# Performance work log

Measured on AMD Instinct MI355X. Metric: run time of the kernel, lower is better.

Reference implementation:

```python
import jax, jax.numpy as jnp
import numpy as np

TAU = 1.0
EPS = 1e-30
LN_EPS = 1e-5


def setup_inputs() -> dict:
    key = jax.random.key(0)
    ks = jax.random.split(key, 5)
    N, E, D_in, D_out = 50000, 800000, 128, 128
    x = jax.random.normal(ks[0], (N, D_in), dtype=jnp.float32)
    edge_src = jax.random.randint(ks[1], (E,), 0, N, dtype=jnp.int64)
    edge_dst = jax.random.randint(ks[2], (E,), 0, N, dtype=jnp.int64)
    W = jax.random.normal(ks[3], (2 * D_in, D_out), dtype=jnp.float32) * (1.0 / np.sqrt(2 * D_in))
    b = jnp.zeros((D_out,), dtype=jnp.float32)
    gamma = jnp.ones((D_out,), dtype=jnp.float32)
    beta = jnp.zeros((D_out,), dtype=jnp.float32)
    return {"x": x, "edge_src": edge_src, "edge_dst": edge_dst, "W": W, "b": b, "gamma": gamma, "beta": beta}


def _scatter_logsumexp(src, index, dim_size):
    # src: [E, D] gathered neighbor features, index: [E] target node ids
    scaled = src.astype(jnp.float32) / TAU
    mx = jax.ops.segment_max(scaled, index, num_segments=dim_size)  # [N, D], -inf for empty
    exp_val = jnp.exp(scaled - mx[index])                            # [E, D]
    sum_exp = jax.ops.segment_sum(exp_val, index, num_segments=dim_size)  # [N, D]
    out = TAU * (mx + jnp.log(jnp.maximum(sum_exp, EPS)))
    deg = jax.ops.segment_sum(jnp.ones_like(index, dtype=jnp.int32), index, num_segments=dim_size)
    return jnp.where((deg > 0)[:, None], out, 0.0)


def reference(x, edge_src, edge_dst, W, b, gamma, beta):
    N = x.shape[0]
    src_feat = x[edge_src]                                  # [E, D] gather
    agg = _scatter_logsumexp(src_feat, edge_dst, N)         # [N, D]
    h = jnp.concatenate([x, agg], axis=-1) @ W + b          # [N, D_out]
    mean = jnp.mean(h, axis=-1, keepdims=True)
    var = jnp.var(h, axis=-1, keepdims=True)
    h = (h - mean) * jax.lax.rsqrt(var + LN_EPS) * gamma + beta
    return jax.nn.relu(h)
```

## Files before the change

### kernel.cpp

```cpp
#include <hip/hip_runtime.h>
#include <math.h>

#define D 128
#define EPS 1e-30f
#define LN_EPS 1e-5f

#define BINSHIFT 9
#define BINW 512
#define NBIN_MAX 128
#define P1_EPB 4096

typedef long long ll;
typedef __attribute__((ext_vector_type(8))) short short8;
typedef __attribute__((ext_vector_type(4))) float f32x4;

__device__ inline unsigned short f2bf(float f) {
    unsigned int u = __float_as_uint(f);
    u += 0x7FFF + ((u >> 16) & 1);
    return (unsigned short)(u >> 16);
}

__device__ inline float bf2f_lo(unsigned int w) { return __uint_as_float(w << 16); }
__device__ inline float bf2f_hi(unsigned int w) { return __uint_as_float(w & 0xFFFF0000u); }

__device__ inline bool idx_is_i64(const void* p, int n_nodes) {
    const ll* q = (const ll*)p;
    bool ok = true;
#pragma unroll
    for (int i = 0; i < 4; ++i) {
        ll v = q[i];
        if (v < 0 || v >= (ll)n_nodes) ok = false;
    }
    return ok;
}

__device__ inline int load_idx(const void* p, ll e, bool is64) {
    return is64 ? (int)((const ll*)p)[e] : ((const int*)p)[e];
}


__global__ __launch_bounds__(256) void k_setup(const float* __restrict__ x,
                                               unsigned short* __restrict__ A,
                                               const float* __restrict__ W,
                                               unsigned short* __restrict__ WT,
                                               const void* __restrict__ edst,
                                               int* __restrict__ bhist,
                                               int N, int E, int PREP_B, int WT_B) {
    __shared__ int hist[NBIN_MAX];
    int b = blockIdx.x, t = threadIdx.x;
    if (b < PREP_B) {
        int i = b * 256 + t;
        if (i < N * 32) {
            int n = i >> 5, c4 = i & 31;
            float4 v = *(const float4*)(x + (ll)n * D + c4 * 4);
            ushort4 o;
            o.x = f2bf(v.x); o.y = f2bf(v.y); o.z = f2bf(v.z); o.w = f2bf(v.w);
            *(ushort4*)(A + (ll)n * 256 + c4 * 4) = o;
        }
        return;
    }
    b -= PREP_B;
    if (b < WT_B) {
        int idx = b * 256 + t;
        int k = idx >> 7, n = idx & 127;
        WT[n * 256 + k] = f2bf(W[idx]);
        return;
    }
    b -= WT_B;
    if (t < NBIN_MAX) hist[t] = 0;
    __syncthreads();
    bool is64 = idx_is_i64(edst, N);
    ll base = (ll)b * P1_EPB;
    int cnt = (int)min((ll)P1_EPB, (ll)E - base);
    for (int i = t; i < cnt; i += 256) {
        int d = load_idx(edst, base + i, is64);
        atomicAdd(&hist[d >> BINSHIFT], 1);
    }
    __syncthreads();
    if (t < NBIN_MAX) bhist[b * NBIN_MAX + t] = hist[t];
}

__global__ __launch_bounds__(NBIN_MAX) void k_binscan(const int* __restrict__ bhist, int EB,
                                                      int* __restrict__ pbase,
                                                      int* __restrict__ pcur,
                                                      int* __restrict__ off, int E, int N) {
    __shared__ int s[NBIN_MAX];
    int t = threadIdx.x;
    int v = 0;
    for (int i = 0; i < EB; ++i) v += bhist[i * NBIN_MAX + t];
    s[t] = v;
    __syncthreads();
    for (int o = 1; o < NBIN_MAX; o <<= 1) {
        int xv = (t >= o) ? s[t - o] : 0;
        __syncthreads();
        s[t] += xv;
        __syncthreads();
    }
    pbase[t] = s[t] - v;
    pcur[t]  = s[t] - v;
    if (t == NBIN_MAX - 1) { pbase[NBIN_MAX] = s[t]; off[N] = E; }
}

__global__ __launch_bounds__(256) void k_pass1b(const void* __restrict__ esrc,
                                                const void* __restrict__ edst,
                                                int* __restrict__ pcur,
                                                unsigned int* __restrict__ pairs,
                                                int E, int N) {
    __shared__ unsigned int sp[P1_EPB];
    __shared__ int hist[NBIN_MAX];
    __shared__ int curs[NBIN_MAX];
    bool is64s = idx_is_i64(esrc, N);
    bool is64d = idx_is_i64(edst, N);
    int t = threadIdx.x;
    if (t < NBIN_MAX) hist[t] = 0;
    __syncthreads();
    ll base = (ll)blockIdx.x * P1_EPB;
    int cnt = (int)min((ll)P1_EPB, (ll)E - base);
    for (int i = t; i < cnt; i += 256) {
        unsigned int s = (unsigned int)load_idx(esrc, base + i, is64s);
        unsigned int d = (unsigned int)load_idx(edst, base + i, is64d);
        sp[i] = (d << 16) | s;
        atomicAdd(&hist[d >> BINSHIFT], 1);
    }
    __syncthreads();
    if (t < NBIN_MAX) curs[t] = hist[t] ? atomicAdd(&pcur[t], hist[t]) : 0;
    __syncthreads();
    for (int i = t; i < cnt; i += 256) {
        unsigned int p = sp[i];
        int b = p >> (16 + BINSHIFT);
        int pos = atomicAdd(&curs[b], 1);
        pairs[pos] = p;
    }
}

__global__ __launch_bounds__(256) void k_pass2(const unsigned int* __restrict__ pairs,
                                               const int* __restrict__ pbase,
                                               int* __restrict__ off,
                                               unsigned short* __restrict__ bucket, int N) {
    __shared__ int dhist[BINW];
    __shared__ int dcur[BINW];
    __shared__ int ssum[256];
    int b = blockIdx.x, t = threadIdx.x;
    int p0 = pbase[b], p1 = pbase[b + 1];
    int n0 = b << BINSHIFT;
    for (int j = t; j < BINW; j += 256) dhist[j] = 0;
    __syncthreads();
    for (int i = p0 + t; i < p1; i += 256)
        atomicAdd(&dhist[(pairs[i] >> 16) & (BINW - 1)], 1);
    __syncthreads();
    int h0 = dhist[2 * t], h1 = dhist[2 * t + 1];
    int loc = h0 + h1;
    ssum[t] = loc;
    __syncthreads();
    for (int o = 1; o < 256; o <<= 1) {
        int xv = (t >= o) ? ssum[t - o] : 0;
        __syncthreads();
        ssum[t] += xv;
        __syncthreads();
    }
    int ex = ssum[t] - loc;
    dcur[2 * t]     = ex;
    dcur[2 * t + 1] = ex + h0;
    __syncthreads();
    int lim = min(BINW, N - n0);
    for (int j = t; j < lim; j += 256) off[n0 + j] = p0 + dcur[j];
    __syncthreads();
    for (int i = p0 + t; i < p1; i += 256) {
        unsigned int p = pairs[i];
        int dl = (p >> 16) & (BINW - 1);
        int pos = p0 + atomicAdd(&dcur[dl], 1);
        bucket[pos] = (unsigned short)(p & 0xFFFFu);
    }
}

__global__ __launch_bounds__(256) void k_aggregate(const int* __restrict__ off,
                                                   const unsigned short* __restrict__ bucket,
                                                   unsigned short* __restrict__ A, int N) {
    __shared__ int sIds[4][64];
    int w = threadIdx.x >> 6, lane = threadIdx.x & 63;
    int n = blockIdx.x * 4 + w;
    if (n >= N) return;
    int start = off[n], end = off[n + 1];
    int sub = lane >> 4, c16 = lane & 15;
    const uint4* A4 = (const uint4*)A;
    float acc[8];
#pragma unroll
    for (int j = 0; j < 8; ++j) acc[j] = 0.f;

    for (int c = start; c < end; c += 64) {
        int cn = min(64, end - c);
        if (lane < cn) sIds[w][lane] = bucket[c + lane];
        int j = sub;
        for (; j + 12 < cn; j += 16) {
            int s0 = sIds[w][j];
            int s1 = sIds[w][j + 4];
            int s2 = sIds[w][j + 8];
            int s3 = sIds[w][j + 12];
            uint4 v0 = A4[(ll)s0 * 32 + c16];
            uint4 v1 = A4[(ll)s1 * 32 + c16];
            uint4 v2 = A4[(ll)s2 * 32 + c16];
            uint4 v3 = A4[(ll)s3 * 32 + c16];
            acc[0] += __expf(bf2f_lo(v0.x)); acc[1] += __expf(bf2f_hi(v0.x));
            acc[2] += __expf(bf2f_lo(v0.y)); acc[3] += __expf(bf2f_hi(v0.y));
            acc[4] += __expf(bf2f_lo(v0.z)); acc[5] += __expf(bf2f_hi(v0.z));
            acc[6] += __expf(bf2f_lo(v0.w)); acc[7] += __expf(bf2f_hi(v0.w));
            acc[0] += __expf(bf2f_lo(v1.x)); acc[1] += __expf(bf2f_hi(v1.x));
            acc[2] += __expf(bf2f_lo(v1.y)); acc[3] += __expf(bf2f_hi(v1.y));
            acc[4] += __expf(bf2f_lo(v1.z)); acc[5] += __expf(bf2f_hi(v1.z));
            acc[6] += __expf(bf2f_lo(v1.w)); acc[7] += __expf(bf2f_hi(v1.w));
            acc[0] += __expf(bf2f_lo(v2.x)); acc[1] += __expf(bf2f_hi(v2.x));
            acc[2] += __expf(bf2f_lo(v2.y)); acc[3] += __expf(bf2f_hi(v2.y));
            acc[4] += __expf(bf2f_lo(v2.z)); acc[5] += __expf(bf2f_hi(v2.z));
            acc[6] += __expf(bf2f_lo(v2.w)); acc[7] += __expf(bf2f_hi(v2.w));
            acc[0] += __expf(bf2f_lo(v3.x)); acc[1] += __expf(bf2f_hi(v3.x));
            acc[2] += __expf(bf2f_lo(v3.y)); acc[3] += __expf(bf2f_hi(v3.y));
            acc[4] += __expf(bf2f_lo(v3.z)); acc[5] += __expf(bf2f_hi(v3.z));
            acc[6] += __expf(bf2f_lo(v3.w)); acc[7] += __expf(bf2f_hi(v3.w));
        }
        for (; j < cn; j += 4) {
            int s0 = sIds[w][j];
            uint4 v0 = A4[(ll)s0 * 32 + c16];
            acc[0] += __expf(bf2f_lo(v0.x)); acc[1] += __expf(bf2f_hi(v0.x));
            acc[2] += __expf(bf2f_lo(v0.y)); acc[3] += __expf(bf2f_hi(v0.y));
            acc[4] += __expf(bf2f_lo(v0.z)); acc[5] += __expf(bf2f_hi(v0.z));
            acc[6] += __expf(bf2f_lo(v0.w)); acc[7] += __expf(bf2f_hi(v0.w));
        }
    }
#pragma unroll
    for (int j = 0; j < 8; ++j) {
        acc[j] += __shfl_xor(acc[j], 16, 64);
        acc[j] += __shfl_xor(acc[j], 32, 64);
    }
    if (sub == 0) {
        int dg = end - start;
        unsigned int o[4];
#pragma unroll
        for (int k = 0; k < 4; ++k) {
            float a0 = (dg > 0) ? __logf(fmaxf(acc[2 * k],     EPS)) : 0.f;
            float a1 = (dg > 0) ? __logf(fmaxf(acc[2 * k + 1], EPS)) : 0.f;
            o[k] = (unsigned int)f2bf(a0) | ((unsigned int)f2bf(a1) << 16);
        }
        *(uint4*)(A + (ll)n * 256 + 128 + c16 * 8) = make_uint4(o[0], o[1], o[2], o[3]);
    }
}

__global__ __launch_bounds__(256) void k_gemm_mfma(
        const unsigned short* __restrict__ A,
        const unsigned short* __restrict__ WT,
        const float* __restrict__ bias,
        const float* __restrict__ gamma,
        const float* __restrict__ beta,
        float* __restrict__ out, int N) {
    __shared__ unsigned char sA[64 * 512];
    __shared__ float2 sPart[2][64];
    int t = threadIdx.x;
    int l = t & 63, w = t >> 6;
    int wr = w >> 1, wc = w & 1;
    int n0 = blockIdx.x * 64;

    const uint4* gA = (const uint4*)(A + (ll)n0 * 256);
#pragma unroll
    for (int i = 0; i < 8; ++i) {
        int c = i * 256 + t;
        int row = c >> 5, cc = c & 31;
        uint4 v = make_uint4(0u, 0u, 0u, 0u);
        if (n0 + row < N) v = gA[row * 32 + cc];
        *(uint4*)(sA + row * 512 + ((cc * 16) ^ ((row & 7) << 4))) = v;
    }
    __syncthreads();

    f32x4 acc[2][4];
#pragma unroll
    for (int m = 0; m < 2; ++m)
#pragma unroll
        for (int n = 0; n < 4; ++n) acc[m][n] = (f32x4){0.f, 0.f, 0.f, 0.f};

    const int lr = l & 15, lk = l >> 4;
    const int aswz = (lr & 7) << 4;
    const unsigned short* wbase = WT + (wc * 64 + lr) * 256 + lk * 8;

#pragma unroll
    for (int ks = 0; ks < 8; ++ks) {
        short8 a[2], b[4];
#pragma unroll
        for (int m = 0; m < 2; ++m) {
            int arow = wr * 32 + m * 16 + lr;
            a[m] = *(const short8*)(sA + arow * 512 + ((ks * 64 + lk * 16) ^ aswz));
        }
#pragma unroll
        for (int n = 0; n < 4; ++n)
            b[n] = *(const short8*)(wbase + n * 16 * 256 + ks * 32);
#pragma unroll
        for (int m = 0; m < 2; ++m)
#pragma unroll
            for (int n = 0; n < 4; ++n)
                acc[m][n] = __builtin_amdgcn_mfma_f32_16x16x32_bf16(a[m], b[n], acc[m][n], 0, 0, 0);
    }

    const int col_base = wc * 64 + lr;
    float bn[4], gn[4], ben[4];
#pragma unroll
    for (int n = 0; n < 4; ++n) {
        int col = col_base + n * 16;
        bn[n] = bias[col]; gn[n] = gamma[col]; ben[n] = beta[col];
    }
#pragma unroll
    for (int m = 0; m < 2; ++m) {
#pragma unroll
        for (int r = 0; r < 4; ++r) {
            float s = 0.f, q = 0.f;
#pragma unroll
            for (int n = 0; n < 4; ++n) {
                float v = acc[m][n][r] + bn[n];
                acc[m][n][r] = v;
                s += v; q += v * v;
            }
#pragma unroll
            for (int o = 1; o < 16; o <<= 1) {
                s += __shfl_xor(s, o, 64);
                q += __shfl_xor(q, o, 64);
            }
            if (lr == 0) {
                int rowl = wr * 32 + m * 16 + lk * 4 + r;
                sPart[wc][rowl] = make_float2(s, q);
            }
        }
    }
    __syncthreads();
#pragma unroll
    for (int m = 0; m < 2; ++m) {
#pragma unroll
        for (int r = 0; r < 4; ++r) {
            int rowl = wr * 32 + m * 16 + lk * 4 + r;
            float2 p0 = sPart[0][rowl], p1 = sPart[1][rowl];
            float ssum = p0.x + p1.x, qsum = p0.y + p1.y;
            float mean = ssum * (1.f / 128.f);
            float var  = qsum * (1.f / 128.f) - mean * mean;
            float rstd = rsqrtf(var + LN_EPS);
            int grow = n0 + rowl;
            if (grow < N) {
                float* op = out + (ll)grow * 128;
#pragma unroll
                for (int n = 0; n < 4; ++n) {
                    float y = (acc[m][n][r] - mean) * rstd * gn[n] + ben[n];
                    op[col_base + n * 16] = fmaxf(y, 0.f);
                }
            }
        }
    }
}


__global__ __launch_bounds__(256) void k_wt(const float* __restrict__ W,
                                            unsigned short* __restrict__ WT) {
    int idx = blockIdx.x * 256 + threadIdx.x;
    int k = idx >> 7, n = idx & 127;
    WT[n * 256 + k] = f2bf(W[idx]);
}

__global__ __launch_bounds__(256) void k_hist(const void* __restrict__ edst,
                                              int* __restrict__ deg, int E, int N) {
    bool is64 = idx_is_i64(edst, N);
    int i = blockIdx.x * 256 + threadIdx.x;
    if (i < E) atomicAdd(&deg[load_idx(edst, i, is64)], 1);
}

__global__ __launch_bounds__(256) void k_scanA(const int* __restrict__ deg,
                                               int* __restrict__ off,
                                               int* __restrict__ bsum, int N) {
    __shared__ int s[256];
    int b = blockIdx.x, t = threadIdx.x;
    int base = b * 1024 + t * 4;
    int v0 = 0, v1 = 0, v2 = 0, v3 = 0;
    if (base + 0 < N) v0 = deg[base + 0];
    if (base + 1 < N) v1 = deg[base + 1];
    if (base + 2 < N) v2 = deg[base + 2];
    if (base + 3 < N) v3 = deg[base + 3];
    int loc = v0 + v1 + v2 + v3;
    s[t] = loc;
    __syncthreads();
    for (int o = 1; o < 256; o <<= 1) {
        int xv = (t >= o) ? s[t - o] : 0;
        __syncthreads();
        s[t] += xv;
        __syncthreads();
    }
    int run = s[t] - loc;
    if (t == 255) bsum[b] = s[255];
    if (base + 0 < N) off[base + 0] = run; run += v0;
    if (base + 1 < N) off[base + 1] = run; run += v1;
    if (base + 2 < N) off[base + 2] = run; run += v2;
    if (base + 3 < N) off[base + 3] = run;
}

__global__ __launch_bounds__(256) void k_scanB(const int* __restrict__ bsum,
                                               int* __restrict__ bbase, int NB) {
    __shared__ int s[256];
    int t = threadIdx.x;
    int v = (t < NB) ? bsum[t] : 0;
    s[t] = v;
    __syncthreads();
    for (int o = 1; o < 256; o <<= 1) {
        int xv = (t >= o) ? s[t - o] : 0;
        __syncthreads();
        s[t] += xv;
        __syncthreads();
    }
    if (t < NB) bbase[t] = s[t] - v;
}

__global__ __launch_bounds__(256) void k_scanC(int* __restrict__ off,
                                               int* __restrict__ cur,
                                               const int* __restrict__ bbase, int N, int E) {
    int b = blockIdx.x, t = threadIdx.x;
    int add = bbase[b];
    int base = b * 1024 + t * 4;
#pragma unroll
    for (int i = 0; i < 4; ++i) {
        int idx = base + i;
        if (idx < N) {
            int o = off[idx] + add;
            off[idx] = o;
            cur[idx] = o;
        }
    }
    if (b == 0 && t == 0) off[N] = E;
}

__global__ __launch_bounds__(256) void k_scatter32(const void* __restrict__ esrc,
                                                   const void* __restrict__ edst,
                                                   int* __restrict__ cur,
                                                   unsigned short* __restrict__ bucket,
                                                   int E, int N) {
    bool is64s = idx_is_i64(esrc, N);
    bool is64d = idx_is_i64(edst, N);
    int i = blockIdx.x * 256 + threadIdx.x;
    if (i < E) {
        int s = load_idx(esrc, i, is64s);
        int d = load_idx(edst, i, is64d);
        int pos = atomicAdd(&cur[d], 1);
        bucket[pos] = (unsigned short)s;
    }
}

__global__ __launch_bounds__(128) void k_aggregate_mid(const float* __restrict__ x,
                                                       const unsigned short* __restrict__ bucket,
                                                       const int* __restrict__ off,
                                                       unsigned short* __restrict__ A, int N) {
    int n = blockIdx.x, t = threadIdx.x;
    int start = __builtin_amdgcn_readfirstlane(off[n]);
    int end   = __builtin_amdgcn_readfirstlane(off[n + 1]);
    float acc = 0.f;
    for (int e = start; e < end; ++e) {
        int s0 = bucket[e];
        acc += __expf(x[(ll)s0 * D + t]);
    }
    float agg = (end > start) ? __logf(fmaxf(acc, EPS)) : 0.f;
    A[(ll)n * 256 + t]       = f2bf(x[(ll)n * D + t]);
    A[(ll)n * 256 + 128 + t] = f2bf(agg);
}


__global__ __launch_bounds__(256) void scatter_expsum(
        const float* __restrict__ x, const void* __restrict__ esrc_raw,
        const void* __restrict__ edst_raw, float* __restrict__ sumexp,
        int* __restrict__ deg, int E, int N) {
    ll tid = (ll)blockIdx.x * blockDim.x + threadIdx.x;
    ll total = (ll)E * 32;
    if (tid >= total) return;
    bool is64 = idx_is_i64(esrc_raw, N);
    ll e = tid >> 5;
    int q = (int)(tid & 31);
    int s = load_idx(esrc_raw, e, is64);
    int d = load_idx(edst_raw, e, is64);
    const float4 v = *reinterpret_cast<const float4*>(x + (ll)s * D + q * 4);
    float* outp = sumexp + (ll)d * D + q * 4;
    atomicAdd(outp + 0, expf(v.x));
    atomicAdd(outp + 1, expf(v.y));
    atomicAdd(outp + 2, expf(v.z));
    atomicAdd(outp + 3, expf(v.w));
    if (q == 0) atomicAdd(deg + d, 1);
}

__global__ __launch_bounds__(128) void gemm_ln_relu_fb(
        const float* __restrict__ x, const float* __restrict__ sumexp,
        const int* __restrict__ deg, const float* __restrict__ W,
        const float* __restrict__ bias, const float* __restrict__ gamma,
        const float* __restrict__ beta, float* __restrict__ out) {
    const int n = blockIdx.x;
    const int t = threadIdx.x;
    __shared__ float v[2 * D];
    __shared__ float s_sum[2], s_sq[2];
    v[t] = x[(ll)n * D + t];
    float se = sumexp[(ll)n * D + t];
    v[D + t] = (deg[n] > 0) ? logf(fmaxf(se, EPS)) : 0.0f;
    __syncthreads();
    float acc = bias[t];
#pragma unroll 8
    for (int k = 0; k < 2 * D; ++k) acc += v[k] * W[k * D + t];
    float sum = acc, sq = acc * acc;
#pragma unroll
    for (int o = 32; o > 0; o >>= 1) {
        sum += __shfl_xor(sum, o, 64);
        sq  += __shfl_xor(sq, o, 64);
    }
    int w = t >> 6;
    if ((t & 63) == 0) { s_sum[w] = sum; s_sq[w] = sq; }
    __syncthreads();
    float mean = (s_sum[0] + s_sum[1]) * (1.0f / D);
    float var  = (s_sq[0] + s_sq[1]) * (1.0f / D) - mean * mean;
    float r = rsqrtf(var + LN_EPS);
    float y = (acc - mean) * r * gamma[t] + beta[t];
    out[(ll)n * D + t] = fmaxf(y, 0.0f);
}


extern "C" void kernel_launch(void* const* d_in, const int* in_sizes, int n_in,
                              void* d_out, int out_size, void* d_ws, size_t ws_size,
                              hipStream_t stream) {
    const float* x     = (const float*)d_in[0];
    const void*  esrc  = d_in[1];
    const void*  edst  = d_in[2];
    const float* W     = (const float*)d_in[3];
    const float* bias  = (const float*)d_in[4];
    const float* gamma = (const float*)d_in[5];
    const float* beta  = (const float*)d_in[6];

    const int E = in_sizes[1];
    const int N = in_sizes[0] / D;
    float* out = (float*)d_out;
    unsigned short* A = (unsigned short*)d_out;

    const int EB = (E + P1_EPB - 1) / P1_EPB;
    const int PREP_B = (N * 32 + 255) / 256;
    const int NBIN = (N + BINW - 1) >> BINSHIFT;

    size_t need_fast = ((size_t)(N + 1) + 129 + 128 + (size_t)EB * NBIN_MAX + (size_t)E) * 4
                     + (size_t)E * 2 + 2 + 65536;
    const int NB = (N + 1023) / 1024;
    size_t need_mid = ((size_t)3 * N + 1 + 512 + 16384) * 4 + (size_t)E * 2 + 2;

    if (N <= 65536 && ws_size >= need_fast) {
        int* off            = (int*)d_ws;
        int* pbase          = off + (N + 1);
        int* pcur           = pbase + 129;
        int* bhist          = pcur + 128;
        unsigned int* pairs = (unsigned int*)(bhist + (size_t)EB * NBIN_MAX);
        unsigned short* bucket = (unsigned short*)(pairs + E);
        unsigned short* wt  = (unsigned short*)((char*)(bucket + E) + (((size_t)(bucket + E)) & 2 ? 2 : 0));

        k_setup<<<PREP_B + 128 + EB, 256, 0, stream>>>(x, A, W, wt, edst, bhist, N, E, PREP_B, 128);
        k_binscan<<<1, NBIN_MAX, 0, stream>>>(bhist, EB, pbase, pcur, off, E, N);
        k_pass1b<<<EB, 256, 0, stream>>>(esrc, edst, pcur, pairs, E, N);
        k_pass2<<<NBIN, 256, 0, stream>>>(pairs, pbase, off, bucket, N);
        k_aggregate<<<(N + 3) / 4, 256, 0, stream>>>(off, bucket, A, N);
        k_gemm_mfma<<<(N + 63) / 64, 256, 0, stream>>>(A, wt, bias, gamma, beta, out, N);
    } else if (N <= 65536 && ws_size >= need_mid && NB <= 256) {
        int* deg    = (int*)d_ws;
        int* off    = deg + N;
        int* cur    = off + (N + 1);
        int* bsum   = cur + N;
        int* bbase  = bsum + 256;
        unsigned short* wt = (unsigned short*)(bbase + 256);
        unsigned short* bucket = wt + 32768;

        hipMemsetAsync(deg, 0, (size_t)N * sizeof(int), stream);
        int eb = (E + 255) / 256;
        k_wt<<<128, 256, 0, stream>>>(W, wt);
        k_hist<<<eb, 256, 0, stream>>>(edst, deg, E, N);
        k_scanA<<<NB, 256, 0, stream>>>(deg, off, bsum, N);
        k_scanB<<<1, 256, 0, stream>>>(bsum, bbase, NB);
        k_scanC<<<NB, 256, 0, stream>>>(off, cur, bbase, N, E);
        k_scatter32<<<eb, 256, 0, stream>>>(esrc, edst, cur, bucket, E, N);
        k_aggregate_mid<<<N, 128, 0, stream>>>(x, bucket, off, A, N);
        k_gemm_mfma<<<(N + 63) / 64, 256, 0, stream>>>(A, wt, bias, gamma, beta, out, N);
    } else {
        float* sumexp = out;
        int* deg = (int*)d_ws;
        hipMemsetAsync(sumexp, 0, (size_t)N * D * sizeof(float), stream);
        hipMemsetAsync(deg, 0, (size_t)N * sizeof(int), stream);
        ll total = (ll)E * 32;
        int blocks = (int)((total + 255) / 256);
        scatter_expsum<<<blocks, 256, 0, stream>>>(x, esrc, edst, sumexp, deg, E, N);
        gemm_ln_relu_fb<<<N, D, 0, stream>>>(x, sumexp, deg, W, bias, gamma, beta, out);
    }
}
```

Before: 143.2 us.

## Fuse neighbor aggregation into MFMA GEMM+LayerNorm kernel, staging A in workspace

Merges the log-sum-exp aggregation kernel into the GEMM/LayerNorm kernel. Each 64-row block gathers neighbor features, computes the aggregate and writes it straight into its shared-memory A tile, then runs the MFMA GEMM. This removes one launch and the global write/read of the aggregated half of A. A now lives in the workspace instead of aliasing the output buffer, since other blocks still gather x rows from A while outputs are written. The cost is lower parallelism during aggregation: 782 blocks each process 16 nodes per wave serially instead of 12.5k small blocks, which risks load imbalance and poorer latency hiding.

```diff
diff --git a/kernel.cpp b/kernel.cpp
--- a/kernel.cpp
+++ b/kernel.cpp
@@ -173,75 +173,291 @@
     }
 }
 
-__global__ __launch_bounds__(256) void k_aggregate(const int* __restrict__ off,
-                                                   const unsigned short* __restrict__ bucket,
-                                                   unsigned short* __restrict__ A, int N) {
+__global__ __launch_bounds__(256) void k_agg_gemm(
+        const unsigned short* __restrict__ A,
+        const int* __restrict__ off,
+        const unsigned short* __restrict__ bucket,
+        const unsigned short* __restrict__ WT,
+        const float* __restrict__ bias,
+        const float* __restrict__ gamma,
+        const float* __restrict__ beta,
+        float* __restrict__ out, int N) {
+    __shared__ unsigned char sA[64 * 512];
+    __shared__ float2 sPart[2][64];
     __shared__ int sIds[4][64];
-    int w = threadIdx.x >> 6, lane = threadIdx.x & 63;
-    int n = blockIdx.x * 4 + w;
-    if (n >= N) return;
-    int start = off[n], end = off[n + 1];
-    int sub = lane >> 4, c16 = lane & 15;
-    const uint4* A4 = (const uint4*)A;
-    float acc[8];
-#pragma unroll
-    for (int j = 0; j < 8; ++j) acc[j] = 0.f;
-
-    for (int c = start; c < end; c += 64) {
-        int cn = min(64, end - c);
-        if (lane < cn) sIds[w][lane] = bucket[c + lane];
-        int j = sub;
-        for (; j + 12 < cn; j += 16) {
-            int s0 = sIds[w][j];
-            int s1 = sIds[w][j + 4];
-            int s2 = sIds[w][j + 8];
-            int s3 = sIds[w][j + 12];
-            uint4 v0 = A4[(ll)s0 * 32 + c16];
-            uint4 v1 = A4[(ll)s1 * 32 + c16];
-            uint4 v2 = A4[(ll)s2 * 32 + c16];
-            uint4 v3 = A4[(ll)s3 * 32 + c16];
-            acc[0] += __expf(bf2f_lo(v0.x)); acc[1] += __expf(bf2f_hi(v0.x));
-            acc[2] += __expf(bf2f_lo(v0.y)); acc[3] += __expf(bf2f_hi(v0.y));
-            acc[4] += __expf(bf2f_lo(v0.z)); acc[5] += __expf(bf2f_hi(v0.z));
-            acc[6] += __expf(bf2f_lo(v0.w)); acc[7] += __expf(bf2f_hi(v0.w));
-            acc[0] += __expf(bf2f_lo(v1.x)); acc[1] += __expf(bf2f_hi(v1.x));
-            acc[2] += __expf(bf2f_lo(v1.y)); acc[3] += __expf(bf2f_hi(v1.y));
-            acc[4] += __expf(bf2f_lo(v1.z)); acc[5] += __expf(bf2f_hi(v1.z));
-            acc[6] += __expf(bf2f_lo(v1.w)); acc[7] += __expf(bf2f_hi(v1.w));
-            acc[0] += __expf(bf2f_lo(v2.x)); acc[1] += __expf(bf2f_hi(v2.x));
-            acc[2] += __expf(bf2f_lo(v2.y)); acc[3] += __expf(bf2f_hi(v2.y));
-            acc[4] += __expf(bf2f_lo(v2.z)); acc[5] += __expf(bf2f_hi(v2.z));
-            acc[6] += __expf(bf2f_lo(v2.w)); acc[7] += __expf(bf2f_hi(v2.w));
-            acc[0] += __expf(bf2f_lo(v3.x)); acc[1] += __expf(bf2f_hi(v3.x));
-            acc[2] += __expf(bf2f_lo(v3.y)); acc[3] += __expf(bf2f_hi(v3.y));
-            acc[4] += __expf(bf2f_lo(v3.z)); acc[5] += __expf(bf2f_hi(v3.z));
-            acc[6] += __expf(bf2f_lo(v3.w)); acc[7] += __expf(bf2f_hi(v3.w));
-        }
-        for (; j < cn; j += 4) {
-            int s0 = sIds[w][j];
-            uint4 v0 = A4[(ll)s0 * 32 + c16];
-            acc[0] += __expf(bf2f_lo(v0.x)); acc[1] += __expf(bf2f_hi(v0.x));
-            acc[2] += __expf(bf2f_lo(v0.y)); acc[3] += __expf(bf2f_hi(v0.y));
-            acc[4] += __expf(bf2f_lo(v0.z)); acc[5] += __expf(bf2f_hi(v0.z));
-            acc[6] += __expf(bf2f_lo(v0.w)); acc[7] += __expf(bf2f_hi(v0.w));
-        }
-    }
-#pragma unroll
-    for (int j = 0; j < 8; ++j) {
-        acc[j] += __shfl_xor(acc[j], 16, 64);
-        acc[j] += __shfl_xor(acc[j], 32, 64);
-    }
-    if (sub == 0) {
-        int dg = end - start;
-        unsigned int o[4];
-#pragma unroll
-        for (int k = 0; k < 4; ++k) {
-            float a0 = (dg > 0) ? __logf(fmaxf(acc[2 * k],     EPS)) : 0.f;
-            float a1 = (dg > 0) ? __logf(fmaxf(acc[2 * k + 1], EPS)) : 0.f;
-            o[k] = (unsigned int)f2bf(a0) | ((unsigned int)f2bf(a1) << 16);
-        }
-        *(uint4*)(A + (ll)n * 256 + 128 + c16 * 8) = make_uint4(o[0], o[1], o[2], o[3]);
-    }
+    int t = threadIdx.x;
+    int l = t & 63, w = t >> 6;
+    int n0 = blockIdx.x * 64;
+
+    const uint4* gA = (const uint4*)A;
+#pragma unroll
+    for (int i = 0; i < 4; ++i) {
+        int c = i * 256 + t;
+        int row = c >> 4;
+        int cc = c & 15;
+        uint4 v = make_uint4(0u, 0u, 0u, 0u);
+        if (n0 + row < N) v = gA[(ll)(n0 + row) * 32 + cc];
+        *(uint4*)(sA + row * 512 + ((cc * 16) ^ ((row & 7) << 4))) = v;
+    }
+
+    int sub = l >> 4, c16 = l & 15;
+    for (int i = 0; i < 16; ++i) {
+        int row = w * 16 + i;
+        int n = n0 + row;
+        if (n >= N) break;
+        int start = off[n], end = off[n + 1];
+        float acc[8];
+#pragma unroll
+        for (int j = 0; j < 8; ++j) acc[j] = 0.f;
+        for (int c = start; c < end; c += 64) {
+            int cn = min(64, end - c);
+            if (l < cn) sIds[w][l] = bucket[c + l];
+            int j = sub;
+            for (; j + 12 < cn; j += 16) {
+                int s0 = sIds[w][j];
+                int s1 = sIds[w][j + 4];
+                int s2 = sIds[w][j + 8];
+                int s3 = sIds[w][j + 12];
+                uint4 v0 = gA[(ll)s0 * 32 + c16];
+                uint4 v1 = gA[(ll)s1 * 32 + c16];
+                uint4 v2 = gA[(ll)s2 * 32 + c16];
+                uint4 v3 = gA[(ll)s3 * 32 + c16];
+                acc[0] += __expf(bf2f_lo(v0.x)); acc[1] += __expf(bf2f_hi(v0.x));
+                acc[2] += __expf(bf2f_lo(v0.y)); acc[3] += __expf(bf2f_hi(v0.y));
+                acc[4] += __expf(bf2f_lo(v0.z)); acc[5] += __expf(bf2f_hi(v0.z));
+                acc[6] += __expf(bf2f_lo(v0.w)); acc[7] += __expf(bf2f_hi(v0.w));
+                acc[0] += __expf(bf2f_lo(v1.x)); acc[1] += __expf(bf2f_hi(v1.x));
+                acc[2] += __expf(bf2f_lo(v1.y)); acc[3] += __expf(bf2f_hi(v1.y));
+                acc[4] += __expf(bf2f_lo(v1.z)); acc[5] += __expf(bf2f_hi(v1.z));
+                acc[6] += __expf(bf2f_lo(v1.w)); acc[7] += __expf(bf2f_hi(v1.w));
+                acc[0] += __expf(bf2f_lo(v2.x)); acc[1] += __expf(bf2f_hi(v2.x));
+                acc[2] += __expf(bf2f_lo(v2.y)); acc[3] += __expf(bf2f_hi(v2.y));
+                acc[4] += __expf(bf2f_lo(v2.z)); acc[5] += __expf(bf2f_hi(v2.z));
+                acc[6] += __expf(bf2f_lo(v2.w)); acc[7] += __expf(bf2f_hi(v2.w));
+                acc[0] += __expf(bf2f_lo(v3.x)); acc[1] += __expf(bf2f_hi(v3.x));
+                acc[2] += __expf(bf2f_lo(v3.y)); acc[3] += __expf(bf2f_hi(v3.y));
+                acc[4] += __expf(bf2f_lo(v3.z)); acc[5] += __expf(bf2f_hi(v3.z));
+                acc[6] += __expf(bf2f_lo(v3.w)); acc[7] += __expf(bf2f_hi(v3.w));
+            }
+            for (; j < cn; j += 4) {
+                int s0 = sIds[w][j];
+                uint4 v0 = gA[(ll)s0 * 32 + c16];
+                acc[0] += __expf(bf2f_lo(v0.x)); acc[1] += __expf(bf2f_hi(v0.x));
+                acc[2] += __expf(bf2f_lo(v0.y)); acc[3] += __expf(bf2f_hi(v0.y));
+                acc[4] += __expf(bf2f_lo(v0.z)); acc[5] += __expf(bf2f_hi(v0.z));
+                acc[6] += __expf(bf2f_lo(v0.w)); acc[7] += __expf(bf2f_hi(v0.w));
+            }
+        }
+#pragma unroll
+        for (int j = 0; j < 8; ++j) {
+            acc[j] += __shfl_xor(acc[j], 16, 64);
+            acc[j] += __shfl_xor(acc[j], 32, 64);
+        }
+        if (sub == 0) {
+            int dg = end - start;
+            unsigned int o[4];
+#pragma unroll
+            for (int k = 0; k < 4; ++k) {
+                float a0 = (dg > 0) ? __logf(fmaxf(acc[2 * k],     EPS)) : 0.f;
+                float a1 = (dg > 0) ? __logf(fmaxf(acc[2 * k + 1], EPS)) : 0.f;
+                o[k] = (unsigned int)f2bf(a0) | ((unsigned int)f2bf(a1) << 16);
+            }
+            *(uint4*)(sA + row * 512 + (((16 + c16) * 16) ^ ((row & 7) << 4))) =
+                make_uint4(o[0], o[1], o[2], o[3]);
+        }
+    }
+    __syncthreads();
+
+    int wr = w >> 1, wc = w & 1;
+    f32x4 acc[2][4];
+#pragma unroll
+    for (int m = 0; m < 2; ++m)
+#pragma unroll
+        for (int n = 0; n < 4; ++n) acc[m][n] = (f32x4){0.f, 0.f, 0.f, 0.f};
+
+    const int lr = l & 15, lk = l >> 4;
+    const int aswz = (lr & 7) << 4;
+    const unsigned short* wbase = WT + (wc * 64 + lr) * 256 + lk * 8;
+
+#pragma unroll
+    for (int ks = 0; ks < 8; ++ks) {
+        short8 a[2], b[4];
+#pragma unroll
+        for (int m = 0; m < 2; ++m) {
+            int arow = wr * 32 + m * 16 + lr;
+            a[m] = *(const short8*)(sA + arow * 512 + ((ks * 64 + lk * 16) ^ aswz));
+        }
+#pragma unroll
+        for (int n = 0; n < 4; ++n)
+            b[n] = *(const short8*)(wbase + n * 16 * 256 + ks * 32);
+#pragma unroll
+        for (int m = 0; m < 2; ++m)
+#pragma unroll
+            for (int n = 0; n < 4; ++n)
+                acc[m][n] = __builtin_amdgcn_mfma_f32_16x16x32_bf16(a[m], b[n], acc[m][n], 0, 0, 0);
+    }
+
+    const int col_base = wc * 64 + lr;
+    float bn[4], gn[4], ben[4];
+#pragma unroll
+    for (int n = 0; n < 4; ++n) {
+        int col = col_base + n * 16;
+        bn[n] = bias[col]; gn[n] = gamma[col]; ben[n] = beta[col];
+    }
+#pragma unroll
+    for (int m = 0; m < 2; ++m) {
+#pragma unroll
+        for (int r = 0; r < 4; ++r) {
+            float s = 0.f, q = 0.f;
+#pragma unroll
+            for (int n = 0; n < 4; ++n) {
+                float v = acc[m][n][r] + bn[n];
+                acc[m][n][r] = v;
+                s += v; q += v * v;
+            }
+#pragma unroll
+            for (int o = 1; o < 16; o <<= 1) {
+                s += __shfl_xor(s, o, 64);
+                q += __shfl_xor(q, o, 64);
+            }
+            if (lr == 0) {
+                int rowl = wr * 32 + m * 16 + lk * 4 + r;
+                sPart[wc][rowl] = make_float2(s, q);
+            }
+        }
+    }
+    __syncthreads();
+#pragma unroll
+    for (int m = 0; m < 2; ++m) {
+#pragma unroll
+        for (int r = 0; r < 4; ++r) {
+            int rowl = wr * 32 + m * 16 + lk * 4 + r;
+            float2 p0 = sPart[0][rowl], p1 = sPart[1][rowl];
+            float ssum = p0.x + p1.x, qsum = p0.y + p1.y;
+            float mean = ssum * (1.f / 128.f);
+            float var  = qsum * (1.f / 128.f) - mean * mean;
+            float rstd = rsqrtf(var + LN_EPS);
+            int grow = n0 + rowl;
+            if (grow < N) {
+                float* op = out + (ll)grow * 128;
+#pragma unroll
+                for (int n = 0; n < 4; ++n) {
+                    float y = (acc[m][n][r] - mean) * rstd * gn[n] + ben[n];
+                    op[col_base + n * 16] = fmaxf(y, 0.f);
+                }
+            }
+        }
+    }
+}
+
+
+__global__ __launch_bounds__(256) void k_wt(const float* __restrict__ W,
+                                            unsigned short* __restrict__ WT) {
+    int idx = blockIdx.x * 256 + threadIdx.x;
+    int k = idx >> 7, n = idx & 127;
+    WT[n * 256 + k] = f2bf(W[idx]);
+}
+
+__global__ __launch_bounds__(256) void k_hist(const void* __restrict__ edst,
+                                              int* __restrict__ deg, int E, int N) {
+    bool is64 = idx_is_i64(edst, N);
+    int i = blockIdx.x * 256 + threadIdx.x;
+    if (i < E) atomicAdd(&deg[load_idx(edst, i, is64)], 1);
+}
+
+__global__ __launch_bounds__(256) void k_scanA(const int* __restrict__ deg,
+                                               int* __restrict__ off,
+                                               int* __restrict__ bsum, int N) {
+    __shared__ int s[256];
+    int b = blockIdx.x, t = threadIdx.x;
+    int base = b * 1024 + t * 4;
+    int v0 = 0, v1 = 0, v2 = 0, v3 = 0;
+    if (base + 0 < N) v0 = deg[base + 0];
+    if (base + 1 < N) v1 = deg[base + 1];
+    if (base + 2 < N) v2 = deg[base + 2];
+    if (base + 3 < N) v3 = deg[base + 3];
+    int loc = v0 + v1 + v2 + v3;
+    s[t] = loc;
+    __syncthreads();
+    for (int o = 1; o < 256; o <<= 1) {
+        int xv = (t >= o) ? s[t - o] : 0;
+        __syncthreads();
+        s[t] += xv;
+        __syncthreads();
+    }
+    int run = s[t] - loc;
+    if (t == 255) bsum[b] = s[255];
+    if (base + 0 < N) off[base + 0] = run; run += v0;
+    if (base + 1 < N) off[base + 1] = run; run += v1;
+    if (base + 2 < N) off[base + 2] = run; run += v2;
+    if (base + 3 < N) off[base + 3] = run;
+}
+
+__global__ __launch_bounds__(256) void k_scanB(const int* __restrict__ bsum,
+                                               int* __restrict__ bbase, int NB) {
+    __shared__ int s[256];
+    int t = threadIdx.x;
+    int v = (t < NB) ? bsum[t] : 0;
+    s[t] = v;
+    __syncthreads();
+    for (int o = 1; o < 256; o <<= 1) {
+        int xv = (t >= o) ? s[t - o] : 0;
+        __syncthreads();
+        s[t] += xv;
+        __syncthreads();
+    }
+    if (t < NB) bbase[t] = s[t] - v;
+}
+
+__global__ __launch_bounds__(256) void k_scanC(int* __restrict__ off,
+                                               int* __restrict__ cur,
+                                               const int* __restrict__ bbase, int N, int E) {
+    int b = blockIdx.x, t = threadIdx.x;
+    int add = bbase[b];
+    int base = b * 1024 + t * 4;
+#pragma unroll
+    for (int i = 0; i < 4; ++i) {
+        int idx = base + i;
+        if (idx < N) {
+            int o = off[idx] + add;
+            off[idx] = o;
+            cur[idx] = o;
+        }
+    }
+    if (b == 0 && t == 0) off[N] = E;
+}
+
+__global__ __launch_bounds__(256) void k_scatter32(const void* __restrict__ esrc,
+                                                   const void* __restrict__ edst,
+                                                   int* __restrict__ cur,
+                                                   unsigned short* __restrict__ bucket,
+                                                   int E, int N) {
+    bool is64s = idx_is_i64(esrc, N);
+    bool is64d = idx_is_i64(edst, N);
+    int i = blockIdx.x * 256 + threadIdx.x;
+    if (i < E) {
+        int s = load_idx(esrc, i, is64s);
+        int d = load_idx(edst, i, is64d);
+        int pos = atomicAdd(&cur[d], 1);
+        bucket[pos] = (unsigned short)s;
+    }
+}
+
+__global__ __launch_bounds__(128) void k_aggregate_mid(const float* __restrict__ x,
+                                                       const unsigned short* __restrict__ bucket,
+                                                       const int* __restrict__ off,
+                                                       unsigned short* __restrict__ A, int N) {
+    int n = blockIdx.x, t = threadIdx.x;
+    int start = __builtin_amdgcn_readfirstlane(off[n]);
+    int end   = __builtin_amdgcn_readfirstlane(off[n + 1]);
+    float acc = 0.f;
+    for (int e = start; e < end; ++e) {
+        int s0 = bucket[e];
+        acc += __expf(x[(ll)s0 * D + t]);
+    }
+    float agg = (end > start) ? __logf(fmaxf(acc, EPS)) : 0.f;
+    A[(ll)n * 256 + t]       = f2bf(x[(ll)n * D + t]);
+    A[(ll)n * 256 + 128 + t] = f2bf(agg);
 }
 
 __global__ __launch_bounds__(256) void k_gemm_mfma(
@@ -348,116 +564,6 @@
             }
         }
     }
-}
-
-
-__global__ __launch_bounds__(256) void k_wt(const float* __restrict__ W,
-                                            unsigned short* __restrict__ WT) {
-    int idx = blockIdx.x * 256 + threadIdx.x;
-    int k = idx >> 7, n = idx & 127;
-    WT[n * 256 + k] = f2bf(W[idx]);
-}
-
-__global__ __launch_bounds__(256) void k_hist(const void* __restrict__ edst,
-                                              int* __restrict__ deg, int E, int N) {
-    bool is64 = idx_is_i64(edst, N);
-    int i = blockIdx.x * 256 + threadIdx.x;
-    if (i < E) atomicAdd(&deg[load_idx(edst, i, is64)], 1);
-}
-
-__global__ __launch_bounds__(256) void k_scanA(const int* __restrict__ deg,
-                                               int* __restrict__ off,
-                                               int* __restrict__ bsum, int N) {
-    __shared__ int s[256];
-    int b = blockIdx.x, t = threadIdx.x;
-    int base = b * 1024 + t * 4;
-    int v0 = 0, v1 = 0, v2 = 0, v3 = 0;
-    if (base + 0 < N) v0 = deg[base + 0];
-    if (base + 1 < N) v1 = deg[base + 1];
-    if (base + 2 < N) v2 = deg[base + 2];
-    if (base + 3 < N) v3 = deg[base + 3];
-    int loc = v0 + v1 + v2 + v3;
-    s[t] = loc;
-    __syncthreads();
-    for (int o = 1; o < 256; o <<= 1) {
-        int xv = (t >= o) ? s[t - o] : 0;
-        __syncthreads();
-        s[t] += xv;
-        __syncthreads();
-    }
-    int run = s[t] - loc;
-    if (t == 255) bsum[b] = s[255];
-    if (base + 0 < N) off[base + 0] = run; run += v0;
-    if (base + 1 < N) off[base + 1] = run; run += v1;
-    if (base + 2 < N) off[base + 2] = run; run += v2;
-    if (base + 3 < N) off[base + 3] = run;
-}
-
-__global__ __launch_bounds__(256) void k_scanB(const int* __restrict__ bsum,
-                                               int* __restrict__ bbase, int NB) {
-    __shared__ int s[256];
-    int t = threadIdx.x;
-    int v = (t < NB) ? bsum[t] : 0;
-    s[t] = v;
-    __syncthreads();
-    for (int o = 1; o < 256; o <<= 1) {
-        int xv = (t >= o) ? s[t - o] : 0;
-        __syncthreads();
-        s[t] += xv;
-        __syncthreads();
-    }
-    if (t < NB) bbase[t] = s[t] - v;
-}
-
-__global__ __launch_bounds__(256) void k_scanC(int* __restrict__ off,
-                                               int* __restrict__ cur,
-                                               const int* __restrict__ bbase, int N, int E) {
-    int b = blockIdx.x, t = threadIdx.x;
-    int add = bbase[b];
-    int base = b * 1024 + t * 4;
-#pragma unroll
-    for (int i = 0; i < 4; ++i) {
-        int idx = base + i;
-        if (idx < N) {
-            int o = off[idx] + add;
-            off[idx] = o;
-            cur[idx] = o;
-        }
-    }
-    if (b == 0 && t == 0) off[N] = E;
-}
-
-__global__ __launch_bounds__(256) void k_scatter32(const void* __restrict__ esrc,
-                                                   const void* __restrict__ edst,
-                                                   int* __restrict__ cur,
-                                                   unsigned short* __restrict__ bucket,
-                                                   int E, int N) {
-    bool is64s = idx_is_i64(esrc, N);
-    bool is64d = idx_is_i64(edst, N);
-    int i = blockIdx.x * 256 + threadIdx.x;
-    if (i < E) {
-        int s = load_idx(esrc, i, is64s);
-        int d = load_idx(edst, i, is64d);
-        int pos = atomicAdd(&cur[d], 1);
-        bucket[pos] = (unsigned short)s;
-    }
-}
-
-__global__ __launch_bounds__(128) void k_aggregate_mid(const float* __restrict__ x,
-                                                       const unsigned short* __restrict__ bucket,
-                                                       const int* __restrict__ off,
-                                                       unsigned short* __restrict__ A, int N) {
-    int n = blockIdx.x, t = threadIdx.x;
-    int start = __builtin_amdgcn_readfirstlane(off[n]);
-    int end   = __builtin_amdgcn_readfirstlane(off[n + 1]);
-    float acc = 0.f;
-    for (int e = start; e < end; ++e) {
-        int s0 = bucket[e];
-        acc += __expf(x[(ll)s0 * D + t]);
-    }
-    float agg = (end > start) ? __logf(fmaxf(acc, EPS)) : 0.f;
-    A[(ll)n * 256 + t]       = f2bf(x[(ll)n * D + t]);
-    A[(ll)n * 256 + 128 + t] = f2bf(agg);
 }
 
 
@@ -529,19 +635,20 @@
     const int E = in_sizes[1];
     const int N = in_sizes[0] / D;
     float* out = (float*)d_out;
-    unsigned short* A = (unsigned short*)d_out;
 
     const int EB = (E + P1_EPB - 1) / P1_EPB;
     const int PREP_B = (N * 32 + 255) / 256;
     const int NBIN = (N + BINW - 1) >> BINSHIFT;
 
-    size_t need_fast = ((size_t)(N + 1) + 129 + 128 + (size_t)EB * NBIN_MAX + (size_t)E) * 4
+    size_t need_fast = (size_t)N * 512
+                     + ((size_t)(N + 1) + 129 + 128 + (size_t)EB * NBIN_MAX + (size_t)E) * 4
                      + (size_t)E * 2 + 2 + 65536;
     const int NB = (N + 1023) / 1024;
     size_t need_mid = ((size_t)3 * N + 1 + 512 + 16384) * 4 + (size_t)E * 2 + 2;
 
     if (N <= 65536 && ws_size >= need_fast) {
-        int* off            = (int*)d_ws;
+        unsigned short* A   = (unsigned short*)d_ws;
+        int* off            = (int*)(A + (size_t)N * 256);
         int* pbase          = off + (N + 1);
         int* pcur           = pbase + 129;
         int* bhist          = pcur + 128;
@@ -553,9 +660,10 @@
         k_binscan<<<1, NBIN_MAX, 0, stream>>>(bhist, EB, pbase, pcur, off, E, N);
         k_pass1b<<<EB, 256, 0, stream>>>(esrc, edst, pcur, pairs, E, N);
         k_pass2<<<NBIN, 256, 0, stream>>>(pairs, pbase, off, bucket, N);
-        k_aggregate<<<(N + 3) / 4, 256, 0, stream>>>(off, bucket, A, N);
-        k_gemm_mfma<<<(N + 63) / 64, 256, 0, stream>>>(A, wt, bias, gamma, beta, out, N);
+        k_agg_gemm<<<(N + 63) / 64, 256, 0, stream>>>(A, off, bucket, wt,
+                                                      bias, gamma, beta, out, N);
     } else if (N <= 65536 && ws_size >= need_mid && NB <= 256) {
+        unsigned short* A = (unsigned short*)d_out;
         int* deg    = (int*)d_ws;
         int* off    = deg + N;
         int* cur    = off + (N + 1);
```

After: 155.1 us. +8.3%, slower.

## Precompute exp(x) per node in bf16 and gather it in aggregation

Applied to the files above, without the earlier changes.

The setup kernel now writes a separate bf16 table of exp(x) per node, so the aggregation kernel gathers precomputed exponentials and only sums them. This drops E*D exponentials in favour of N*D and gathers from a compact 256-byte row instead of the 512-byte stride of the A buffer. The aggregation loop is also unrolled to 8 gathers per iteration for more memory-level parallelism. The cost is an extra N*D bf16 workspace buffer written during setup, rounding exp to bf16 before summation, and no max-subtraction, which risks overflow for large inputs.

```diff
diff --git a/kernel.cpp b/kernel.cpp
--- a/kernel.cpp
+++ b/kernel.cpp
@@ -41,6 +41,7 @@
 
 __global__ __launch_bounds__(256) void k_setup(const float* __restrict__ x,
                                                unsigned short* __restrict__ A,
+                                               unsigned short* __restrict__ expx,
                                                const float* __restrict__ W,
                                                unsigned short* __restrict__ WT,
                                                const void* __restrict__ edst,
@@ -56,6 +57,10 @@
             ushort4 o;
             o.x = f2bf(v.x); o.y = f2bf(v.y); o.z = f2bf(v.z); o.w = f2bf(v.w);
             *(ushort4*)(A + (ll)n * 256 + c4 * 4) = o;
+            ushort4 e;
+            e.x = f2bf(__expf(v.x)); e.y = f2bf(__expf(v.y));
+            e.z = f2bf(__expf(v.z)); e.w = f2bf(__expf(v.w));
+            *(ushort4*)(expx + (ll)n * D + c4 * 4) = e;
         }
         return;
     }
@@ -175,6 +180,7 @@
 
 __global__ __launch_bounds__(256) void k_aggregate(const int* __restrict__ off,
                                                    const unsigned short* __restrict__ bucket,
+                                                   const unsigned short* __restrict__ expx,
                                                    unsigned short* __restrict__ A, int N) {
     __shared__ int sIds[4][64];
     int w = threadIdx.x >> 6, lane = threadIdx.x & 63;
@@ -182,7 +188,7 @@
     if (n >= N) return;
     int start = off[n], end = off[n + 1];
     int sub = lane >> 4, c16 = lane & 15;
-    const uint4* A4 = (const uint4*)A;
+    const uint4* E4 = (const uint4*)expx;
     float acc[8];
 #pragma unroll
     for (int j = 0; j < 8; ++j) acc[j] = 0.f;
@@ -191,39 +197,35 @@
         int cn = min(64, end - c);
         if (lane < cn) sIds[w][lane] = bucket[c + lane];
         int j = sub;
-        for (; j + 12 < cn; j += 16) {
+        for (; j + 28 < cn; j += 32) {
             int s0 = sIds[w][j];
             int s1 = sIds[w][j + 4];
             int s2 = sIds[w][j + 8];
             int s3 = sIds[w][j + 12];
-            uint4 v0 = A4[(ll)s0 * 32 + c16];
-            uint4 v1 = A4[(ll)s1 * 32 + c16];
-            uint4 v2 = A4[(ll)s2 * 32 + c16];
-            uint4 v3 = A4[(ll)s3 * 32 + c16];
-            acc[0] += __expf(bf2f_lo(v0.x)); acc[1] += __expf(bf2f_hi(v0.x));
-            acc[2] += __expf(bf2f_lo(v0.y)); acc[3] += __expf(bf2f_hi(v0.y));
-            acc[4] += __expf(bf2f_lo(v0.z)); acc[5] += __expf(bf2f_hi(v0.z));
-            acc[6] += __expf(bf2f_lo(v0.w)); acc[7] += __expf(bf2f_hi(v0.w));
-            acc[0] += __expf(bf2f_lo(v1.x)); acc[1] += __expf(bf2f_hi(v1.x));
-            acc[2] += __expf(bf2f_lo(v1.y)); acc[3] += __expf(bf2f_hi(v1.y));
-            acc[4] += __expf(bf2f_lo(v1.z)); acc[5] += __expf(bf2f_hi(v1.z));
-            acc[6] += __expf(bf2f_lo(v1.w)); acc[7] += __expf(bf2f_hi(v1.w));
-            acc[0] += __expf(bf2f_lo(v2.x)); acc[1] += __expf(bf2f_hi(v2.x));
-            acc[2] += __expf(bf2f_lo(v2.y)); acc[3] += __expf(bf2f_hi(v2.y));
-            acc[4] += __expf(bf2f_lo(v2.z)); acc[5] += __expf(bf2f_hi(v2.z));
-            acc[6] += __expf(bf2f_lo(v2.w)); acc[7] += __expf(bf2f_hi(v2.w));
-            acc[0] += __expf(bf2f_lo(v3.x)); acc[1] += __expf(bf2f_hi(v3.x));
-            acc[2] += __expf(bf2f_lo(v3.y)); acc[3] += __expf(bf2f_hi(v3.y));
-            acc[4] += __expf(bf2f_lo(v3.z)); acc[5] += __expf(bf2f_hi(v3.z));
-            acc[6] += __expf(bf2f_lo(v3.w)); acc[7] += __expf(bf2f_hi(v3.w));
+            int s4 = sIds[w][j + 16];
+            int s5 = sIds[w][j + 20];
+            int s6 = sIds[w][j + 24];
+            int s7 = sIds[w][j + 28];
+            uint4 v0 = E4[(ll)s0 * 16 + c16];
+            uint4 v1 = E4[(ll)s1 * 16 + c16];
+            uint4 v2 = E4[(ll)s2 * 16 + c16];
+            uint4 v3 = E4[(ll)s3 * 16 + c16];
+            uint4 v4 = E4[(ll)s4 * 16 + c16];
+            uint4 v5 = E4[(ll)s5 * 16 + c16];
+            uint4 v6 = E4[(ll)s6 * 16 + c16];
+            uint4 v7 = E4[(ll)s7 * 16 + c16];
+#define ACC(v) \
+            acc[0] += bf2f_lo(v.x); acc[1] += bf2f_hi(v.x); \
+            acc[2] += bf2f_lo(v.y); acc[3] += bf2f_hi(v.y); \
+            acc[4] += bf2f_lo(v.z); acc[5] += bf2f_hi(v.z); \
+            acc[6] += bf2f_lo(v.w); acc[7] += bf2f_hi(v.w);
+            ACC(v0) ACC(v1) ACC(v2) ACC(v3) ACC(v4) ACC(v5) ACC(v6) ACC(v7)
         }
         for (; j < cn; j += 4) {
             int s0 = sIds[w][j];
-            uint4 v0 = A4[(ll)s0 * 32 + c16];
-            acc[0] += __expf(bf2f_lo(v0.x)); acc[1] += __expf(bf2f_hi(v0.x));
-            acc[2] += __expf(bf2f_lo(v0.y)); acc[3] += __expf(bf2f_hi(v0.y));
-            acc[4] += __expf(bf2f_lo(v0.z)); acc[5] += __expf(bf2f_hi(v0.z));
-            acc[6] += __expf(bf2f_lo(v0.w)); acc[7] += __expf(bf2f_hi(v0.w));
+            uint4 v0 = E4[(ll)s0 * 16 + c16];
+            ACC(v0)
+#undef ACC
         }
     }
 #pragma unroll
@@ -535,25 +537,28 @@
     const int PREP_B = (N * 32 + 255) / 256;
     const int NBIN = (N + BINW - 1) >> BINSHIFT;
 
-    size_t need_fast = ((size_t)(N + 1) + 129 + 128 + (size_t)EB * NBIN_MAX + (size_t)E) * 4
-                     + (size_t)E * 2 + 2 + 65536;
+    size_t need_fast = (size_t)N * 256
+                     + ((size_t)(N + 1) + 129 + 128 + (size_t)EB * NBIN_MAX + (size_t)E) * 4
+                     + 65536 + (size_t)E * 2 + 64;
     const int NB = (N + 1023) / 1024;
     size_t need_mid = ((size_t)3 * N + 1 + 512 + 16384) * 4 + (size_t)E * 2 + 2;
 
     if (N <= 65536 && ws_size >= need_fast) {
-        int* off            = (int*)d_ws;
-        int* pbase          = off + (N + 1);
-        int* pcur           = pbase + 129;
-        int* bhist          = pcur + 128;
-        unsigned int* pairs = (unsigned int*)(bhist + (size_t)EB * NBIN_MAX);
-        unsigned short* bucket = (unsigned short*)(pairs + E);
-        unsigned short* wt  = (unsigned short*)((char*)(bucket + E) + (((size_t)(bucket + E)) & 2 ? 2 : 0));
-
-        k_setup<<<PREP_B + 128 + EB, 256, 0, stream>>>(x, A, W, wt, edst, bhist, N, E, PREP_B, 128);
+        unsigned short* expx = (unsigned short*)d_ws;
+        int* off             = (int*)(expx + (size_t)N * 128);
+        int* pbase           = off + (N + 1);
+        int* pcur            = pbase + 129;
+        int* bhist           = pcur + 128;
+        unsigned int* pairs  = (unsigned int*)(bhist + (size_t)EB * NBIN_MAX);
+        unsigned short* wt   = (unsigned short*)((((size_t)(pairs + E)) + 15) & ~(size_t)15);
+        unsigned short* bucket = wt + 32768;
+
+        k_setup<<<PREP_B + 128 + EB, 256, 0, stream>>>(x, A, expx, W, wt, edst, bhist,
+                                                       N, E, PREP_B, 128);
         k_binscan<<<1, NBIN_MAX, 0, stream>>>(bhist, EB, pbase, pcur, off, E, N);
         k_pass1b<<<EB, 256, 0, stream>>>(esrc, edst, pcur, pairs, E, N);
         k_pass2<<<NBIN, 256, 0, stream>>>(pairs, pbase, off, bucket, N);
-        k_aggregate<<<(N + 3) / 4, 256, 0, stream>>>(off, bucket, A, N);
+        k_aggregate<<<(N + 3) / 4, 256, 0, stream>>>(off, bucket, expx, A, N);
         k_gemm_mfma<<<(N + 63) / 64, 256, 0, stream>>>(A, wt, bias, gamma, beta, out, N);
     } else if (N <= 65536 && ws_size >= need_mid && NB <= 256) {
         int* deg    = (int*)d_ws;
```

Result: slower. 150.0 us (+4.8%).
